# Kernel optimization log

Hardware: AMD Instinct MI355X
Metric: run time of the kernel (lower is better)

The kernel has to match this reference:

```python
import jax, jax.numpy as jnp
import numpy as np

B, S, E = 2, 2048, 1024
H = 16
D = E // H
LAYER_IDX = 2.0
MASKED_BIAS = -10000.0


def setup_inputs() -> dict:
    key = jax.random.key(0)
    k1, k2, k3 = jax.random.split(key, 3)
    hidden_state = jax.random.normal(k1, (B, S, E), dtype=jnp.float32)
    w_attn = jax.random.normal(k2, (E, 3 * E), dtype=jnp.float32) * 0.2
    b_attn = jnp.zeros((3 * E,), dtype=jnp.float32)
    w_proj = jax.random.normal(k3, (E, E), dtype=jnp.float32) * 0.2
    b_proj = jnp.zeros((E,), dtype=jnp.float32)
    return {"hidden_state": hidden_state, "w_attn": w_attn, "b_attn": b_attn,
            "w_proj": w_proj, "b_proj": b_proj}


def reference(hidden_state, w_attn, b_attn, w_proj, b_proj):
    b, s, e = hidden_state.shape
    # c_attn: Conv1D == x @ W + b, then split into q, k, v
    qkv = hidden_state @ w_attn + b_attn          # [b, s, 3E]
    q, k, v = jnp.split(qkv, 3, axis=-1)
    # split heads -> [b, H, s, D]
    def split_heads(t):
        return t.reshape(b, s, H, D).transpose(0, 2, 1, 3)
    q, k, v = split_heads(q), split_heads(k), split_heads(v)
    # QK^T scaled by sqrt(d_head) then by layer_idx
    scores = jnp.einsum("bhqd,bhkd->bhqk", q, k)
    scores = scores / jnp.asarray(D ** 0.5, scores.dtype)
    scores = scores / LAYER_IDX
    # causal mask with masked_bias fill (-10000.0), matching bias buffer slice
    causal = jnp.tril(jnp.ones((s, s), dtype=bool))  # [s, s]
    scores = jnp.where(causal[None, None, :, :], scores, jnp.asarray(MASKED_BIAS, scores.dtype))
    attn = jax.nn.softmax(scores, axis=-1)
    out = jnp.einsum("bhqk,bhkd->bhqd", attn, v)   # [b, H, s, D]
    # merge heads
    out = out.transpose(0, 2, 1, 3).reshape(b, s, e)
    # c_proj
    return out @ w_proj + b_proj
```

## Files before the change

### kernel.cpp

```cpp
#include <hip/hip_runtime.h>
#include <cstddef>
#include <cstdint>

#define B_DIM   2
#define S_LEN   2048
#define EMB     1024
#define NH      16
#define HD      64
#define QKV_N   3072
#define MROWS   (B_DIM * S_LEN)

using half8  = __attribute__((ext_vector_type(8))) _Float16;
using half4  = __attribute__((ext_vector_type(4))) _Float16;
using f32x4  = __attribute__((ext_vector_type(4))) float;

#if defined(__has_builtin)
#if __has_builtin(__builtin_amdgcn_global_load_lds)
#define HAS_GLL 1
#endif
#endif

__device__ __forceinline__ void stage16(const _Float16* g, _Float16* lds_base, int lane)
{
#ifdef HAS_GLL
    (void)lane;
    __builtin_amdgcn_global_load_lds(
        (const __attribute__((address_space(1))) unsigned int*)g,
        (__attribute__((address_space(3))) unsigned int*)lds_base, 16, 0, 0);
#else
    *(half8*)(lds_base + lane * 8) = *(const half8*)g;
#endif
}

__global__ __launch_bounds__(256)
void prep_all(const float* __restrict__ hidden, const float* __restrict__ w_attn,
              const float* __restrict__ w_proj, _Float16* __restrict__ hidden_h,
              _Float16* __restrict__ wattn_t, _Float16* __restrict__ wproj_t)
{
    const int bid = blockIdx.x, t = threadIdx.x;
    if (bid < 4096) {
        int i = bid * 1024 + t * 4;
        float4 v = *(const float4*)(hidden + i);
        half4 h = { (_Float16)v.x, (_Float16)v.y, (_Float16)v.z, (_Float16)v.w };
        *(half4*)(hidden_h + i) = h;
        return;
    }
    __shared__ float T[32][33];
    const float* W; _Float16* Wt; int N, bx, by;
    if (bid < 7168) {
        int t2 = bid - 4096; bx = t2 % 96; by = t2 / 96; W = w_attn; Wt = wattn_t; N = QKV_N;
    } else {
        int t3 = bid - 7168; bx = t3 & 31; by = t3 >> 5; W = w_proj; Wt = wproj_t; N = EMB;
    }
    const int n0 = bx * 32, k0 = by * 32;
    const int r = t >> 3, c4 = (t & 7) * 4;
    float4 w = *(const float4*)(W + (size_t)(k0 + r) * N + n0 + c4);
    T[r][c4 + 0] = w.x; T[r][c4 + 1] = w.y;
    T[r][c4 + 2] = w.z; T[r][c4 + 3] = w.w;
    __syncthreads();
    half4 h = { (_Float16)T[c4 + 0][r], (_Float16)T[c4 + 1][r],
                (_Float16)T[c4 + 2][r], (_Float16)T[c4 + 3][r] };
    *(half4*)(Wt + (size_t)(n0 + r) * EMB + k0 + c4) = h;
}

template <int MT, int MINW, bool OUT_F16, bool FUSE_VT>
__global__ __launch_bounds__(256, MINW)
void hgemm_lds(const _Float16* __restrict__ X, const _Float16* __restrict__ Wt,
               const float* __restrict__ bias, void* __restrict__ Cout,
               _Float16* __restrict__ vt, int M, int N, int K)
{
    constexpr int BM = MT * 32;
    constexpr int ACALLS = BM / 32;
    __shared__ _Float16 As[BM][64];
    __shared__ _Float16 Bs[128][64];

    const int tid  = threadIdx.x;
    const int wave = tid >> 6, lane = tid & 63;
    const int quad = lane >> 4, l15 = lane & 15;
    const int wm = (wave >> 1) * (MT * 16);
    const int wn = (wave & 1) * 64;
    const int m0 = blockIdx.y * BM, n0 = blockIdx.x * 128;

    const int srow = lane >> 3;
    const int scol = ((lane & 7) ^ srow) * 8;

    const _Float16* xg[ACALLS];
#pragma unroll
    for (int c = 0; c < ACALLS; ++c)
        xg[c] = X + (size_t)(m0 + wave * (BM / 4) + c * 8 + srow) * K + scol;
    const _Float16* wg[4];
#pragma unroll
    for (int c = 0; c < 4; ++c)
        wg[c] = Wt + (size_t)(n0 + wave * 32 + c * 8 + srow) * K + scol;

    f32x4 acc[MT][4] = {};
    const int sx = l15 & 7;

    for (int k0 = 0; k0 < K; k0 += 64) {
#pragma unroll
        for (int c = 0; c < ACALLS; ++c)
            stage16(xg[c] + k0, &As[wave * (BM / 4) + c * 8][0], lane);
#pragma unroll
        for (int c = 0; c < 4; ++c)
            stage16(wg[c] + k0, &Bs[wave * 32 + c * 8][0], lane);
        __syncthreads();

#pragma unroll
        for (int cc = 0; cc < 2; ++cc) {
            half8 af[MT], bf[4];
#pragma unroll
            for (int mt = 0; mt < MT; ++mt)
                af[mt] = *(const half8*)&As[wm + mt * 16 + l15][(((cc * 4 + quad) ^ sx)) * 8];
#pragma unroll
            for (int nt = 0; nt < 4; ++nt)
                bf[nt] = *(const half8*)&Bs[wn + nt * 16 + l15][(((cc * 4 + quad) ^ sx)) * 8];
#pragma unroll
            for (int mt = 0; mt < MT; ++mt)
#pragma unroll
                for (int nt = 0; nt < 4; ++nt)
                    acc[mt][nt] = __builtin_amdgcn_mfma_f32_16x16x32_f16(
                        af[mt], bf[nt], acc[mt][nt], 0, 0, 0);
        }
        __syncthreads();
    }

    if (FUSE_VT && n0 >= 2 * EMB) {
#pragma unroll
        for (int nt = 0; nt < 4; ++nt) {
            const int c  = n0 + wn + nt * 16 + l15;
            const float bv = bias[c];
            const int vcol = c - 2 * EMB;
            const int hh = vcol >> 6, dd = vcol & 63;
#pragma unroll
            for (int mt = 0; mt < MT; ++mt) {
                const int r = m0 + wm + mt * 16 + quad * 4;
                const int bb = r >> 11, ss = r & 2047;
                half4 o = { (_Float16)(acc[mt][nt][0] + bv), (_Float16)(acc[mt][nt][1] + bv),
                            (_Float16)(acc[mt][nt][2] + bv), (_Float16)(acc[mt][nt][3] + bv) };
                *(half4*)(vt + ((size_t)(bb * NH + hh) * HD + dd) * S_LEN + ss) = o;
            }
        }
        return;
    }

#pragma unroll
    for (int nt = 0; nt < 4; ++nt) {
        const int c = n0 + wn + nt * 16 + l15;
        const float bv = bias[c];
#pragma unroll
        for (int mt = 0; mt < MT; ++mt)
#pragma unroll
            for (int reg = 0; reg < 4; ++reg) {
                const int r = m0 + wm + mt * 16 + quad * 4 + reg;
                const float v = acc[mt][nt][reg] + bv;
                if (OUT_F16)
                    ((_Float16*)Cout)[(size_t)r * N + c] = (_Float16)v;
                else
                    ((float*)Cout)[(size_t)r * N + c] = v;
            }
    }
}

__global__ __launch_bounds__(256, 2)
void attn_fa_mfma7(const _Float16* __restrict__ qkv,
                   const _Float16* __restrict__ vt,
                   _Float16* __restrict__ outh)
{
    __shared__ _Float16 Ks[128][64];
    __shared__ _Float16 Vs[64][128];

    const int n   = blockIdx.x;
    const int xcd = n & 7, g = (n >> 3) & 3, j = n >> 5;
    const int bh  = xcd * 4 + g;
    const int qta = j, qtb = 31 - j;
    const int b = bh >> 4, h = bh & 15;

    const int tid  = threadIdx.x;
    const int wave = tid >> 6, lane = tid & 63;
    const int quad = lane >> 4, l15 = lane & 15;
    const size_t row0 = (size_t)b * S_LEN;

    const _Float16 qscale = (_Float16)0.0901684400555602f;
    half8 qfa[2], qfb[2];
    {
        const _Float16* qpa = qkv + (row0 + qta * 64 + wave * 16 + l15) * QKV_N + h * HD + quad * 8;
        const _Float16* qpb = qkv + (row0 + qtb * 64 + wave * 16 + l15) * QKV_N + h * HD + quad * 8;
#pragma unroll
        for (int c = 0; c < 2; ++c) {
            half8 qa = *(const half8*)(qpa + c * 32);
            half8 qb = *(const half8*)(qpb + c * 32);
#pragma unroll
            for (int j2 = 0; j2 < 8; ++j2) { qa[j2] *= qscale; qb[j2] *= qscale; }
            qfa[c] = qa; qfb[c] = qb;
        }
    }

    f32x4 o_a[4] = {}, o_b[4] = {};
    float m_a = -1e30f, l_a = 0.0f, m_b = -1e30f, l_b = 0.0f;

    const int ksrow = lane >> 3;
    const int kscol = ((lane & 7) ^ ksrow) * 8;
    const int vsrow = lane >> 4;
    const _Float16* vbase = vt + (size_t)bh * HD * S_LEN;
    const int sxk = l15 & 7;

    auto softmax_pack = [&](f32x4 (&st)[8], half4 (&pf)[8], float& m_i, float& l_i,
                            f32x4 (&o_acc)[4]) {
        float rm = fmaxf(fmaxf(st[0][0], st[0][1]), fmaxf(st[0][2], st[0][3]));
#pragma unroll
        for (int nt = 1; nt < 8; ++nt) {
            rm = fmaxf(rm, fmaxf(st[nt][0], st[nt][1]));
            rm = fmaxf(rm, fmaxf(st[nt][2], st[nt][3]));
        }
        rm = fmaxf(rm, __shfl_xor(rm, 16));
        rm = fmaxf(rm, __shfl_xor(rm, 32));
        const float mnew = fmaxf(m_i, rm);
        if (__ballot(mnew > m_i)) {
            const float alpha = __builtin_amdgcn_exp2f(m_i - mnew);
            l_i *= alpha;
#pragma unroll
            for (int dt = 0; dt < 4; ++dt)
#pragma unroll
                for (int reg = 0; reg < 4; ++reg) o_acc[dt][reg] *= alpha;
        }
        m_i = mnew;
        float rs = 0.0f;
#pragma unroll
        for (int nt = 0; nt < 8; ++nt) {
            float p0 = __builtin_amdgcn_exp2f(st[nt][0] - mnew);
            float p1 = __builtin_amdgcn_exp2f(st[nt][1] - mnew);
            float p2 = __builtin_amdgcn_exp2f(st[nt][2] - mnew);
            float p3 = __builtin_amdgcn_exp2f(st[nt][3] - mnew);
            rs += (p0 + p1) + (p2 + p3);
            pf[nt] = half4{ (_Float16)p0, (_Float16)p1, (_Float16)p2, (_Float16)p3 };
        }
        rs += __shfl_xor(rs, 16);
        rs += __shfl_xor(rs, 32);
        l_i += rs;
    };

    const int ktNa = (qta + 2) >> 1;
    const int ktNb = (qtb + 2) >> 1;

    for (int kt = 0; kt < ktNb; ++kt) {
        __syncthreads();
        {
            const _Float16* kbase = qkv + (row0 + kt * 128) * QKV_N + EMB + h * HD;
#pragma unroll
            for (int c = 0; c < 4; ++c) {
                const int r0 = wave * 32 + c * 8;
                stage16(kbase + (size_t)(r0 + ksrow) * QKV_N + kscol, &Ks[r0][0], lane);
            }
#pragma unroll
            for (int c = 0; c < 4; ++c) {
                const int r0 = wave * 16 + c * 4;
                const int sgv = ((lane & 15) ^ (c * 4 + vsrow)) * 8;
                stage16(vbase + (size_t)(r0 + vsrow) * S_LEN + kt * 128 + sgv, &Vs[r0][0], lane);
            }
        }
        __syncthreads();

        if (kt < ktNa) {
            f32x4 sa[8] = {}, sb[8] = {};
#pragma unroll
            for (int c = 0; c < 2; ++c)
#pragma unroll
                for (int nt = 0; nt < 8; ++nt) {
                    half8 kf = *(const half8*)&Ks[nt * 16 + l15][((c * 4 + quad) ^ sxk) * 8];
                    sa[nt] = __builtin_amdgcn_mfma_f32_16x16x32_f16(kf, qfa[c], sa[nt], 0, 0, 0);
                    sb[nt] = __builtin_amdgcn_mfma_f32_16x16x32_f16(kf, qfb[c], sb[nt], 0, 0, 0);
                }
            if (kt == ktNa - 1) {
                const int q = qta * 64 + wave * 16 + l15;
#pragma unroll
                for (int nt = 0; nt < 8; ++nt) {
                    const int ks = kt * 128 + nt * 16 + quad * 4;
#pragma unroll
                    for (int reg = 0; reg < 4; ++reg)
                        if (ks + reg > q) sa[nt][reg] = -1e30f;
                }
            }
            half4 pfa[8], pfb[8];
            softmax_pack(sa, pfa, m_a, l_a, o_a);
            softmax_pack(sb, pfb, m_b, l_b, o_b);
#pragma unroll
            for (int nt = 0; nt < 8; ++nt)
#pragma unroll
                for (int dt = 0; dt < 4; ++dt) {
                    const int pg = ((2 * nt + (quad >> 1)) ^ l15) * 8 + (quad & 1) * 4;
                    half4 vf = *(const half4*)&Vs[dt * 16 + l15][pg];
                    o_a[dt] = __builtin_amdgcn_mfma_f32_16x16x16f16(vf, pfa[nt], o_a[dt], 0, 0, 0);
                    o_b[dt] = __builtin_amdgcn_mfma_f32_16x16x16f16(vf, pfb[nt], o_b[dt], 0, 0, 0);
                }
        } else {
            f32x4 sb[8] = {};
#pragma unroll
            for (int c = 0; c < 2; ++c)
#pragma unroll
                for (int nt = 0; nt < 8; ++nt) {
                    half8 kf = *(const half8*)&Ks[nt * 16 + l15][((c * 4 + quad) ^ sxk) * 8];
                    sb[nt] = __builtin_amdgcn_mfma_f32_16x16x32_f16(kf, qfb[c], sb[nt], 0, 0, 0);
                }
            if (kt == ktNb - 1) {
                const int q = qtb * 64 + wave * 16 + l15;
#pragma unroll
                for (int nt = 0; nt < 8; ++nt) {
                    const int ks = kt * 128 + nt * 16 + quad * 4;
#pragma unroll
                    for (int reg = 0; reg < 4; ++reg)
                        if (ks + reg > q) sb[nt][reg] = -1e30f;
                }
            }
            half4 pfb[8];
            softmax_pack(sb, pfb, m_b, l_b, o_b);
#pragma unroll
            for (int nt = 0; nt < 8; ++nt)
#pragma unroll
                for (int dt = 0; dt < 4; ++dt) {
                    const int pg = ((2 * nt + (quad >> 1)) ^ l15) * 8 + (quad & 1) * 4;
                    half4 vf = *(const half4*)&Vs[dt * 16 + l15][pg];
                    o_b[dt] = __builtin_amdgcn_mfma_f32_16x16x16f16(vf, pfb[nt], o_b[dt], 0, 0, 0);
                }
        }
    }

    {
        const float inv = 1.0f / l_a;
        const size_t r = row0 + qta * 64 + wave * 16 + l15;
#pragma unroll
        for (int dt = 0; dt < 4; ++dt) {
            half4 o = { (_Float16)(o_a[dt][0] * inv), (_Float16)(o_a[dt][1] * inv),
                        (_Float16)(o_a[dt][2] * inv), (_Float16)(o_a[dt][3] * inv) };
            *(half4*)(outh + r * EMB + h * HD + dt * 16 + quad * 4) = o;
        }
    }
    {
        const float inv = 1.0f / l_b;
        const size_t r = row0 + qtb * 64 + wave * 16 + l15;
#pragma unroll
        for (int dt = 0; dt < 4; ++dt) {
            half4 o = { (_Float16)(o_b[dt][0] * inv), (_Float16)(o_b[dt][1] * inv),
                        (_Float16)(o_b[dt][2] * inv), (_Float16)(o_b[dt][3] * inv) };
            *(half4*)(outh + r * EMB + h * HD + dt * 16 + quad * 4) = o;
        }
    }
}

extern "C" void kernel_launch(void* const* d_in, const int* in_sizes, int n_in,
                              void* d_out, int out_size, void* d_ws, size_t ws_size,
                              hipStream_t stream)
{
    const float* hidden = (const float*)d_in[0];
    const float* w_attn = (const float*)d_in[1];
    const float* b_attn = (const float*)d_in[2];
    const float* w_proj = (const float*)d_in[3];
    const float* b_proj = (const float*)d_in[4];

    _Float16* hidden_h = (_Float16*)d_ws;
    _Float16* wattn_t  = hidden_h + (size_t)MROWS * EMB;
    _Float16* wproj_t  = wattn_t + (size_t)EMB * QKV_N;
    _Float16* qkv_h    = wproj_t + (size_t)EMB * EMB;
    _Float16* attn_h   = qkv_h + (size_t)MROWS * QKV_N;
    _Float16* vt       = attn_h + (size_t)MROWS * EMB;

    prep_all<<<8192, 256, 0, stream>>>(hidden, w_attn, w_proj,
                                       hidden_h, wattn_t, wproj_t);

    hgemm_lds<4, 3, true, true><<<dim3(QKV_N / 128, MROWS / 128), 256, 0, stream>>>(
        hidden_h, wattn_t, b_attn, qkv_h, vt, MROWS, QKV_N, EMB);

    attn_fa_mfma7<<<dim3(512), 256, 0, stream>>>(qkv_h, vt, attn_h);

    hgemm_lds<2, 4, false, false><<<dim3(EMB / 128, MROWS / 64), 256, 0, stream>>>(
        attn_h, wproj_t, b_proj, d_out, nullptr, MROWS, EMB, EMB);
}
```

Before: 170.3 us.

## Double-buffer K/V tiles in attention and raise wave priority around MFMA blocks

The attention kernel now keeps two LDS buffers each for K and V. It issues the global-to-LDS staging of tile kt+1 right after the barrier and before computing on tile kt, which removes one barrier per iteration and overlaps load latency with MFMA work. It also wraps the QK and PV MFMA loops in s_setprio to favour matrix-issuing waves. The cost is doubled LDS use, 64KB per block, which could limit occupancy, and correctness relies on the barrier draining the outstanding async loads.

```diff
diff --git a/kernel.cpp b/kernel.cpp
--- a/kernel.cpp
+++ b/kernel.cpp
@@ -162,12 +162,12 @@
 }
 
 __global__ __launch_bounds__(256, 2)
-void attn_fa_mfma7(const _Float16* __restrict__ qkv,
+void attn_fa_mfma8(const _Float16* __restrict__ qkv,
                    const _Float16* __restrict__ vt,
                    _Float16* __restrict__ outh)
 {
-    __shared__ _Float16 Ks[128][64];
-    __shared__ _Float16 Vs[64][128];
+    __shared__ _Float16 Ks[2][128][64];
+    __shared__ _Float16 Vs[2][64][128];
 
     const int n   = blockIdx.x;
     const int xcd = n & 7, g = (n >> 3) & 3, j = n >> 5;
@@ -203,6 +203,21 @@
     const int vsrow = lane >> 4;
     const _Float16* vbase = vt + (size_t)bh * HD * S_LEN;
     const int sxk = l15 & 7;
+
+    auto stage_tile = [&](int kt, int nb) {
+        const _Float16* kbase = qkv + (row0 + kt * 128) * QKV_N + EMB + h * HD;
+#pragma unroll
+        for (int c = 0; c < 4; ++c) {
+            const int r0 = wave * 32 + c * 8;
+            stage16(kbase + (size_t)(r0 + ksrow) * QKV_N + kscol, &Ks[nb][r0][0], lane);
+        }
+#pragma unroll
+        for (int c = 0; c < 4; ++c) {
+            const int r0 = wave * 16 + c * 4;
+            const int sgv = ((lane & 15) ^ (c * 4 + vsrow)) * 8;
+            stage16(vbase + (size_t)(r0 + vsrow) * S_LEN + kt * 128 + sgv, &Vs[nb][r0][0], lane);
+        }
+    };
 
     auto softmax_pack = [&](f32x4 (&st)[8], half4 (&pf)[8], float& m_i, float& l_i,
                             f32x4 (&o_acc)[4]) {
@@ -242,34 +257,26 @@
     const int ktNa = (qta + 2) >> 1;
     const int ktNb = (qtb + 2) >> 1;
 
+    stage_tile(0, 0);
+
     for (int kt = 0; kt < ktNb; ++kt) {
+        const int cur = kt & 1;
         __syncthreads();
-        {
-            const _Float16* kbase = qkv + (row0 + kt * 128) * QKV_N + EMB + h * HD;
-#pragma unroll
-            for (int c = 0; c < 4; ++c) {
-                const int r0 = wave * 32 + c * 8;
-                stage16(kbase + (size_t)(r0 + ksrow) * QKV_N + kscol, &Ks[r0][0], lane);
-            }
-#pragma unroll
-            for (int c = 0; c < 4; ++c) {
-                const int r0 = wave * 16 + c * 4;
-                const int sgv = ((lane & 15) ^ (c * 4 + vsrow)) * 8;
-                stage16(vbase + (size_t)(r0 + vsrow) * S_LEN + kt * 128 + sgv, &Vs[r0][0], lane);
-            }
-        }
-        __syncthreads();
+        if (kt + 1 < ktNb)
+            stage_tile(kt + 1, cur ^ 1);
 
         if (kt < ktNa) {
             f32x4 sa[8] = {}, sb[8] = {};
+            __builtin_amdgcn_s_setprio(1);
 #pragma unroll
             for (int c = 0; c < 2; ++c)
 #pragma unroll
                 for (int nt = 0; nt < 8; ++nt) {
-                    half8 kf = *(const half8*)&Ks[nt * 16 + l15][((c * 4 + quad) ^ sxk) * 8];
+                    half8 kf = *(const half8*)&Ks[cur][nt * 16 + l15][((c * 4 + quad) ^ sxk) * 8];
                     sa[nt] = __builtin_amdgcn_mfma_f32_16x16x32_f16(kf, qfa[c], sa[nt], 0, 0, 0);
                     sb[nt] = __builtin_amdgcn_mfma_f32_16x16x32_f16(kf, qfb[c], sb[nt], 0, 0, 0);
                 }
+            __builtin_amdgcn_s_setprio(0);
             if (kt == ktNa - 1) {
                 const int q = qta * 64 + wave * 16 + l15;
 #pragma unroll
@@ -283,24 +290,28 @@
             half4 pfa[8], pfb[8];
             softmax_pack(sa, pfa, m_a, l_a, o_a);
             softmax_pack(sb, pfb, m_b, l_b, o_b);
+            __builtin_amdgcn_s_setprio(1);
 #pragma unroll
             for (int nt = 0; nt < 8; ++nt)
 #pragma unroll
                 for (int dt = 0; dt < 4; ++dt) {
                     const int pg = ((2 * nt + (quad >> 1)) ^ l15) * 8 + (quad & 1) * 4;
-                    half4 vf = *(const half4*)&Vs[dt * 16 + l15][pg];
+                    half4 vf = *(const half4*)&Vs[cur][dt * 16 + l15][pg];
                     o_a[dt] = __builtin_amdgcn_mfma_f32_16x16x16f16(vf, pfa[nt], o_a[dt], 0, 0, 0);
                     o_b[dt] = __builtin_amdgcn_mfma_f32_16x16x16f16(vf, pfb[nt], o_b[dt], 0, 0, 0);
                 }
+            __builtin_amdgcn_s_setprio(0);
         } else {
             f32x4 sb[8] = {};
+            __builtin_amdgcn_s_setprio(1);
 #pragma unroll
             for (int c = 0; c < 2; ++c)
 #pragma unroll
                 for (int nt = 0; nt < 8; ++nt) {
-                    half8 kf = *(const half8*)&Ks[nt * 16 + l15][((c * 4 + quad) ^ sxk) * 8];
+                    half8 kf = *(const half8*)&Ks[cur][nt * 16 + l15][((c * 4 + quad) ^ sxk) * 8];
                     sb[nt] = __builtin_amdgcn_mfma_f32_16x16x32_f16(kf, qfb[c], sb[nt], 0, 0, 0);
                 }
+            __builtin_amdgcn_s_setprio(0);
             if (kt == ktNb - 1) {
                 const int q = qtb * 64 + wave * 16 + l15;
 #pragma unroll
@@ -313,14 +324,16 @@
             }
             half4 pfb[8];
             softmax_pack(sb, pfb, m_b, l_b, o_b);
+            __builtin_amdgcn_s_setprio(1);
 #pragma unroll
             for (int nt = 0; nt < 8; ++nt)
 #pragma unroll
                 for (int dt = 0; dt < 4; ++dt) {
                     const int pg = ((2 * nt + (quad >> 1)) ^ l15) * 8 + (quad & 1) * 4;
-                    half4 vf = *(const half4*)&Vs[dt * 16 + l15][pg];
+                    half4 vf = *(const half4*)&Vs[cur][dt * 16 + l15][pg];
                     o_b[dt] = __builtin_amdgcn_mfma_f32_16x16x16f16(vf, pfb[nt], o_b[dt], 0, 0, 0);
                 }
+            __builtin_amdgcn_s_setprio(0);
         }
     }
 
@@ -369,7 +382,7 @@
     hgemm_lds<4, 3, true, true><<<dim3(QKV_N / 128, MROWS / 128), 256, 0, stream>>>(
         hidden_h, wattn_t, b_attn, qkv_h, vt, MROWS, QKV_N, EMB);
 
-    attn_fa_mfma7<<<dim3(512), 256, 0, stream>>>(qkv_h, vt, attn_h);
+    attn_fa_mfma8<<<dim3(512), 256, 0, stream>>>(qkv_h, vt, attn_h);
 
     hgemm_lds<2, 4, false, false><<<dim3(EMB / 128, MROWS / 64), 256, 0, stream>>>(
         attn_h, wproj_t, b_proj, d_out, nullptr, MROWS, EMB, EMB);
```

New measurement: 173.9 us. +2.1%, slower.

## Double-buffer K/V LDS tiles in causal flash-attention kernel

Applied to the files above, without the earlier changes.

Adds a second pair of K/V shared-memory buffers and restructures the key-tile loop into a ping-pong schedule. The next tile's global-to-LDS staging is issued before the current tile's MFMA and softmax work, so load latency can hide behind compute, and one of the two barriers per tile is removed. The cost is twice the LDS per block (64 KB), which may limit occupancy, plus a slightly more complex loop with an early break for odd tile counts.

```diff
diff --git a/kernel.cpp b/kernel.cpp
--- a/kernel.cpp
+++ b/kernel.cpp
@@ -162,12 +162,14 @@
 }
 
 __global__ __launch_bounds__(256, 2)
-void attn_fa_mfma7(const _Float16* __restrict__ qkv,
+void attn_fa_mfma9(const _Float16* __restrict__ qkv,
                    const _Float16* __restrict__ vt,
                    _Float16* __restrict__ outh)
 {
-    __shared__ _Float16 Ks[128][64];
-    __shared__ _Float16 Vs[64][128];
+    __shared__ _Float16 Ks0[128][64];
+    __shared__ _Float16 Vs0[64][128];
+    __shared__ _Float16 Ks1[128][64];
+    __shared__ _Float16 Vs1[64][128];
 
     const int n   = blockIdx.x;
     const int xcd = n & 7, g = (n >> 3) & 3, j = n >> 5;
@@ -203,6 +205,24 @@
     const int vsrow = lane >> 4;
     const _Float16* vbase = vt + (size_t)bh * HD * S_LEN;
     const int sxk = l15 & 7;
+
+    const int ktNa = (qta + 2) >> 1;
+    const int ktNb = (qtb + 2) >> 1;
+
+    auto stage_tile = [&](int kt, _Float16 (&K)[128][64], _Float16 (&V)[64][128]) {
+        const _Float16* kbase = qkv + (row0 + kt * 128) * QKV_N + EMB + h * HD;
+#pragma unroll
+        for (int c = 0; c < 4; ++c) {
+            const int r0 = wave * 32 + c * 8;
+            stage16(kbase + (size_t)(r0 + ksrow) * QKV_N + kscol, &K[r0][0], lane);
+        }
+#pragma unroll
+        for (int c = 0; c < 4; ++c) {
+            const int r0 = wave * 16 + c * 4;
+            const int sgv = ((lane & 15) ^ (c * 4 + vsrow)) * 8;
+            stage16(vbase + (size_t)(r0 + vsrow) * S_LEN + kt * 128 + sgv, &V[r0][0], lane);
+        }
+    };
 
     auto softmax_pack = [&](f32x4 (&st)[8], half4 (&pf)[8], float& m_i, float& l_i,
                             f32x4 (&o_acc)[4]) {
@@ -239,34 +259,14 @@
         l_i += rs;
     };
 
-    const int ktNa = (qta + 2) >> 1;
-    const int ktNb = (qtb + 2) >> 1;
-
-    for (int kt = 0; kt < ktNb; ++kt) {
-        __syncthreads();
-        {
-            const _Float16* kbase = qkv + (row0 + kt * 128) * QKV_N + EMB + h * HD;
-#pragma unroll
-            for (int c = 0; c < 4; ++c) {
-                const int r0 = wave * 32 + c * 8;
-                stage16(kbase + (size_t)(r0 + ksrow) * QKV_N + kscol, &Ks[r0][0], lane);
-            }
-#pragma unroll
-            for (int c = 0; c < 4; ++c) {
-                const int r0 = wave * 16 + c * 4;
-                const int sgv = ((lane & 15) ^ (c * 4 + vsrow)) * 8;
-                stage16(vbase + (size_t)(r0 + vsrow) * S_LEN + kt * 128 + sgv, &Vs[r0][0], lane);
-            }
-        }
-        __syncthreads();
-
+    auto compute_tile = [&](int kt, _Float16 (&K)[128][64], _Float16 (&V)[64][128]) {
         if (kt < ktNa) {
             f32x4 sa[8] = {}, sb[8] = {};
 #pragma unroll
             for (int c = 0; c < 2; ++c)
 #pragma unroll
                 for (int nt = 0; nt < 8; ++nt) {
-                    half8 kf = *(const half8*)&Ks[nt * 16 + l15][((c * 4 + quad) ^ sxk) * 8];
+                    half8 kf = *(const half8*)&K[nt * 16 + l15][((c * 4 + quad) ^ sxk) * 8];
                     sa[nt] = __builtin_amdgcn_mfma_f32_16x16x32_f16(kf, qfa[c], sa[nt], 0, 0, 0);
                     sb[nt] = __builtin_amdgcn_mfma_f32_16x16x32_f16(kf, qfb[c], sb[nt], 0, 0, 0);
                 }
@@ -288,7 +288,7 @@
 #pragma unroll
                 for (int dt = 0; dt < 4; ++dt) {
                     const int pg = ((2 * nt + (quad >> 1)) ^ l15) * 8 + (quad & 1) * 4;
-                    half4 vf = *(const half4*)&Vs[dt * 16 + l15][pg];
+                    half4 vf = *(const half4*)&V[dt * 16 + l15][pg];
                     o_a[dt] = __builtin_amdgcn_mfma_f32_16x16x16f16(vf, pfa[nt], o_a[dt], 0, 0, 0);
                     o_b[dt] = __builtin_amdgcn_mfma_f32_16x16x16f16(vf, pfb[nt], o_b[dt], 0, 0, 0);
                 }
@@ -298,7 +298,7 @@
             for (int c = 0; c < 2; ++c)
 #pragma unroll
                 for (int nt = 0; nt < 8; ++nt) {
-                    half8 kf = *(const half8*)&Ks[nt * 16 + l15][((c * 4 + quad) ^ sxk) * 8];
+                    half8 kf = *(const half8*)&K[nt * 16 + l15][((c * 4 + quad) ^ sxk) * 8];
                     sb[nt] = __builtin_amdgcn_mfma_f32_16x16x32_f16(kf, qfb[c], sb[nt], 0, 0, 0);
                 }
             if (kt == ktNb - 1) {
@@ -318,10 +318,25 @@
 #pragma unroll
                 for (int dt = 0; dt < 4; ++dt) {
                     const int pg = ((2 * nt + (quad >> 1)) ^ l15) * 8 + (quad & 1) * 4;
-                    half4 vf = *(const half4*)&Vs[dt * 16 + l15][pg];
+                    half4 vf = *(const half4*)&V[dt * 16 + l15][pg];
                     o_b[dt] = __builtin_amdgcn_mfma_f32_16x16x16f16(vf, pfb[nt], o_b[dt], 0, 0, 0);
                 }
         }
+    };
+
+    stage_tile(0, Ks0, Vs0);
+
+    for (int kt = 0; kt < ktNb; kt += 2) {
+        __syncthreads();
+        if (kt + 1 < ktNb)
+            stage_tile(kt + 1, Ks1, Vs1);
+        compute_tile(kt, Ks0, Vs0);
+
+        if (kt + 1 >= ktNb) break;
+        __syncthreads();
+        if (kt + 2 < ktNb)
+            stage_tile(kt + 2, Ks0, Vs0);
+        compute_tile(kt + 1, Ks1, Vs1);
     }
 
     {
@@ -369,7 +384,7 @@
     hgemm_lds<4, 3, true, true><<<dim3(QKV_N / 128, MROWS / 128), 256, 0, stream>>>(
         hidden_h, wattn_t, b_attn, qkv_h, vt, MROWS, QKV_N, EMB);
 
-    attn_fa_mfma7<<<dim3(512), 256, 0, stream>>>(qkv_h, vt, attn_h);
+    attn_fa_mfma9<<<dim3(512), 256, 0, stream>>>(qkv_h, vt, attn_h);
 
     hgemm_lds<2, 4, false, false><<<dim3(EMB / 128, MROWS / 64), 256, 0, stream>>>(
         attn_h, wproj_t, b_proj, d_out, nullptr, MROWS, EMB, EMB);
```

Measured after the change: 170.6 us. About the same (+0.2%).

## Split paired-query-tile attention blocks into one tile per block with interleaved ordering

Applied to the files above, without the earlier changes.

The attention kernel previously had each block process two complementary query tiles (j and 31-j) sharing K/V loads. It now assigns one 64-row query tile per block, doubles the grid to 1024 blocks, and uses an interleaved tile ordering so heavy and light causal tiles are mixed across the dispatch. Launch bounds rise to 4 blocks per CU to raise occupancy now that register pressure is halved. The trade-off is that each K/V tile is loaded from global memory twice as often, since tiles no longer share staged K/V.

```diff
diff --git a/kernel.cpp b/kernel.cpp
--- a/kernel.cpp
+++ b/kernel.cpp
@@ -161,18 +161,19 @@
     }
 }
 
-__global__ __launch_bounds__(256, 2)
-void attn_fa_mfma7(const _Float16* __restrict__ qkv,
-                   const _Float16* __restrict__ vt,
-                   _Float16* __restrict__ outh)
+__global__ __launch_bounds__(256, 4)
+void attn_fa_mfma10(const _Float16* __restrict__ qkv,
+                    const _Float16* __restrict__ vt,
+                    _Float16* __restrict__ outh)
 {
     __shared__ _Float16 Ks[128][64];
     __shared__ _Float16 Vs[64][128];
 
     const int n   = blockIdx.x;
     const int xcd = n & 7, g = (n >> 3) & 3, j = n >> 5;
+    const int t   = j & 7, s = j >> 3;
+    const int qt  = (s & 1) ? (31 - 2 * t - (s >> 1)) : (2 * t + (s >> 1));
     const int bh  = xcd * 4 + g;
-    const int qta = j, qtb = 31 - j;
     const int b = bh >> 4, h = bh & 15;
 
     const int tid  = threadIdx.x;
@@ -181,22 +182,20 @@
     const size_t row0 = (size_t)b * S_LEN;
 
     const _Float16 qscale = (_Float16)0.0901684400555602f;
-    half8 qfa[2], qfb[2];
+    half8 qf[2];
     {
-        const _Float16* qpa = qkv + (row0 + qta * 64 + wave * 16 + l15) * QKV_N + h * HD + quad * 8;
-        const _Float16* qpb = qkv + (row0 + qtb * 64 + wave * 16 + l15) * QKV_N + h * HD + quad * 8;
+        const _Float16* qp = qkv + (row0 + qt * 64 + wave * 16 + l15) * QKV_N + h * HD + quad * 8;
 #pragma unroll
         for (int c = 0; c < 2; ++c) {
-            half8 qa = *(const half8*)(qpa + c * 32);
-            half8 qb = *(const half8*)(qpb + c * 32);
-#pragma unroll
-            for (int j2 = 0; j2 < 8; ++j2) { qa[j2] *= qscale; qb[j2] *= qscale; }
-            qfa[c] = qa; qfb[c] = qb;
-        }
-    }
-
-    f32x4 o_a[4] = {}, o_b[4] = {};
-    float m_a = -1e30f, l_a = 0.0f, m_b = -1e30f, l_b = 0.0f;
+            half8 q = *(const half8*)(qp + c * 32);
+#pragma unroll
+            for (int j2 = 0; j2 < 8; ++j2) q[j2] *= qscale;
+            qf[c] = q;
+        }
+    }
+
+    f32x4 o_acc[4] = {};
+    float m_i = -1e30f, l_i = 0.0f;
 
     const int ksrow = lane >> 3;
     const int kscol = ((lane & 7) ^ ksrow) * 8;
@@ -204,45 +203,9 @@
     const _Float16* vbase = vt + (size_t)bh * HD * S_LEN;
     const int sxk = l15 & 7;
 
-    auto softmax_pack = [&](f32x4 (&st)[8], half4 (&pf)[8], float& m_i, float& l_i,
-                            f32x4 (&o_acc)[4]) {
-        float rm = fmaxf(fmaxf(st[0][0], st[0][1]), fmaxf(st[0][2], st[0][3]));
-#pragma unroll
-        for (int nt = 1; nt < 8; ++nt) {
-            rm = fmaxf(rm, fmaxf(st[nt][0], st[nt][1]));
-            rm = fmaxf(rm, fmaxf(st[nt][2], st[nt][3]));
-        }
-        rm = fmaxf(rm, __shfl_xor(rm, 16));
-        rm = fmaxf(rm, __shfl_xor(rm, 32));
-        const float mnew = fmaxf(m_i, rm);
-        if (__ballot(mnew > m_i)) {
-            const float alpha = __builtin_amdgcn_exp2f(m_i - mnew);
-            l_i *= alpha;
-#pragma unroll
-            for (int dt = 0; dt < 4; ++dt)
-#pragma unroll
-                for (int reg = 0; reg < 4; ++reg) o_acc[dt][reg] *= alpha;
-        }
-        m_i = mnew;
-        float rs = 0.0f;
-#pragma unroll
-        for (int nt = 0; nt < 8; ++nt) {
-            float p0 = __builtin_amdgcn_exp2f(st[nt][0] - mnew);
-            float p1 = __builtin_amdgcn_exp2f(st[nt][1] - mnew);
-            float p2 = __builtin_amdgcn_exp2f(st[nt][2] - mnew);
-            float p3 = __builtin_amdgcn_exp2f(st[nt][3] - mnew);
-            rs += (p0 + p1) + (p2 + p3);
-            pf[nt] = half4{ (_Float16)p0, (_Float16)p1, (_Float16)p2, (_Float16)p3 };
-        }
-        rs += __shfl_xor(rs, 16);
-        rs += __shfl_xor(rs, 32);
-        l_i += rs;
-    };
-
-    const int ktNa = (qta + 2) >> 1;
-    const int ktNb = (qtb + 2) >> 1;
-
-    for (int kt = 0; kt < ktNb; ++kt) {
+    const int ktN = (qt + 2) >> 1;
+
+    for (int kt = 0; kt < ktN; ++kt) {
         __syncthreads();
         {
             const _Float16* kbase = qkv + (row0 + kt * 128) * QKV_N + EMB + h * HD;
@@ -260,87 +223,77 @@
         }
         __syncthreads();
 
-        if (kt < ktNa) {
-            f32x4 sa[8] = {}, sb[8] = {};
-#pragma unroll
-            for (int c = 0; c < 2; ++c)
-#pragma unroll
-                for (int nt = 0; nt < 8; ++nt) {
-                    half8 kf = *(const half8*)&Ks[nt * 16 + l15][((c * 4 + quad) ^ sxk) * 8];
-                    sa[nt] = __builtin_amdgcn_mfma_f32_16x16x32_f16(kf, qfa[c], sa[nt], 0, 0, 0);
-                    sb[nt] = __builtin_amdgcn_mfma_f32_16x16x32_f16(kf, qfb[c], sb[nt], 0, 0, 0);
-                }
-            if (kt == ktNa - 1) {
-                const int q = qta * 64 + wave * 16 + l15;
-#pragma unroll
-                for (int nt = 0; nt < 8; ++nt) {
-                    const int ks = kt * 128 + nt * 16 + quad * 4;
-#pragma unroll
-                    for (int reg = 0; reg < 4; ++reg)
-                        if (ks + reg > q) sa[nt][reg] = -1e30f;
-                }
-            }
-            half4 pfa[8], pfb[8];
-            softmax_pack(sa, pfa, m_a, l_a, o_a);
-            softmax_pack(sb, pfb, m_b, l_b, o_b);
-#pragma unroll
-            for (int nt = 0; nt < 8; ++nt)
-#pragma unroll
-                for (int dt = 0; dt < 4; ++dt) {
-                    const int pg = ((2 * nt + (quad >> 1)) ^ l15) * 8 + (quad & 1) * 4;
-                    half4 vf = *(const half4*)&Vs[dt * 16 + l15][pg];
-                    o_a[dt] = __builtin_amdgcn_mfma_f32_16x16x16f16(vf, pfa[nt], o_a[dt], 0, 0, 0);
-                    o_b[dt] = __builtin_amdgcn_mfma_f32_16x16x16f16(vf, pfb[nt], o_b[dt], 0, 0, 0);
-                }
-        } else {
-            f32x4 sb[8] = {};
-#pragma unroll
-            for (int c = 0; c < 2; ++c)
-#pragma unroll
-                for (int nt = 0; nt < 8; ++nt) {
-                    half8 kf = *(const half8*)&Ks[nt * 16 + l15][((c * 4 + quad) ^ sxk) * 8];
-                    sb[nt] = __builtin_amdgcn_mfma_f32_16x16x32_f16(kf, qfb[c], sb[nt], 0, 0, 0);
-                }
-            if (kt == ktNb - 1) {
-                const int q = qtb * 64 + wave * 16 + l15;
-#pragma unroll
-                for (int nt = 0; nt < 8; ++nt) {
-                    const int ks = kt * 128 + nt * 16 + quad * 4;
-#pragma unroll
-                    for (int reg = 0; reg < 4; ++reg)
-                        if (ks + reg > q) sb[nt][reg] = -1e30f;
-                }
-            }
-            half4 pfb[8];
-            softmax_pack(sb, pfb, m_b, l_b, o_b);
-#pragma unroll
-            for (int nt = 0; nt < 8; ++nt)
-#pragma unroll
-                for (int dt = 0; dt < 4; ++dt) {
-                    const int pg = ((2 * nt + (quad >> 1)) ^ l15) * 8 + (quad & 1) * 4;
-                    half4 vf = *(const half4*)&Vs[dt * 16 + l15][pg];
-                    o_b[dt] = __builtin_amdgcn_mfma_f32_16x16x16f16(vf, pfb[nt], o_b[dt], 0, 0, 0);
-                }
-        }
+        f32x4 st[8] = {};
+#pragma unroll
+        for (int c = 0; c < 2; ++c)
+#pragma unroll
+            for (int nt = 0; nt < 8; ++nt) {
+                half8 kf = *(const half8*)&Ks[nt * 16 + l15][((c * 4 + quad) ^ sxk) * 8];
+                st[nt] = __builtin_amdgcn_mfma_f32_16x16x32_f16(kf, qf[c], st[nt], 0, 0, 0);
+            }
+        if (kt == ktN - 1) {
+            const int q = qt * 64 + wave * 16 + l15;
+#pragma unroll
+            for (int nt = 0; nt < 8; ++nt) {
+                const int ks = kt * 128 + nt * 16 + quad * 4;
+#pragma unroll
+                for (int reg = 0; reg < 4; ++reg)
+                    if (ks + reg > q) st[nt][reg] = -1e30f;
+            }
+        }
+
+        half4 pf[8];
+        {
+            float rm = fmaxf(fmaxf(st[0][0], st[0][1]), fmaxf(st[0][2], st[0][3]));
+#pragma unroll
+            for (int nt = 1; nt < 8; ++nt) {
+                rm = fmaxf(rm, fmaxf(st[nt][0], st[nt][1]));
+                rm = fmaxf(rm, fmaxf(st[nt][2], st[nt][3]));
+            }
+            rm = fmaxf(rm, __shfl_xor(rm, 16));
+            rm = fmaxf(rm, __shfl_xor(rm, 32));
+            const float mnew = fmaxf(m_i, rm);
+            if (__ballot(mnew > m_i)) {
+                const float alpha = __builtin_amdgcn_exp2f(m_i - mnew);
+                l_i *= alpha;
+#pragma unroll
+                for (int dt = 0; dt < 4; ++dt)
+#pragma unroll
+                    for (int reg = 0; reg < 4; ++reg) o_acc[dt][reg] *= alpha;
+            }
+            m_i = mnew;
+            float rs = 0.0f;
+#pragma unroll
+            for (int nt = 0; nt < 8; ++nt) {
+                float p0 = __builtin_amdgcn_exp2f(st[nt][0] - mnew);
+                float p1 = __builtin_amdgcn_exp2f(st[nt][1] - mnew);
+                float p2 = __builtin_amdgcn_exp2f(st[nt][2] - mnew);
+                float p3 = __builtin_amdgcn_exp2f(st[nt][3] - mnew);
+                rs += (p0 + p1) + (p2 + p3);
+                pf[nt] = half4{ (_Float16)p0, (_Float16)p1, (_Float16)p2, (_Float16)p3 };
+            }
+            rs += __shfl_xor(rs, 16);
+            rs += __shfl_xor(rs, 32);
+            l_i += rs;
+        }
+
+#pragma unroll
+        for (int nt = 0; nt < 8; ++nt)
+#pragma unroll
+            for (int dt = 0; dt < 4; ++dt) {
+                const int pg = ((2 * nt + (quad >> 1)) ^ l15) * 8 + (quad & 1) * 4;
+                half4 vf = *(const half4*)&Vs[dt * 16 + l15][pg];
+                o_acc[dt] = __builtin_amdgcn_mfma_f32_16x16x16f16(vf, pf[nt], o_acc[dt], 0, 0, 0);
+            }
     }
 
     {
-        const float inv = 1.0f / l_a;
-        const size_t r = row0 + qta * 64 + wave * 16 + l15;
+        const float inv = 1.0f / l_i;
+        const size_t r = row0 + qt * 64 + wave * 16 + l15;
 #pragma unroll
         for (int dt = 0; dt < 4; ++dt) {
-            half4 o = { (_Float16)(o_a[dt][0] * inv), (_Float16)(o_a[dt][1] * inv),
-                        (_Float16)(o_a[dt][2] * inv), (_Float16)(o_a[dt][3] * inv) };
-            *(half4*)(outh + r * EMB + h * HD + dt * 16 + quad * 4) = o;
-        }
-    }
-    {
-        const float inv = 1.0f / l_b;
-        const size_t r = row0 + qtb * 64 + wave * 16 + l15;
-#pragma unroll
-        for (int dt = 0; dt < 4; ++dt) {
-            half4 o = { (_Float16)(o_b[dt][0] * inv), (_Float16)(o_b[dt][1] * inv),
-                        (_Float16)(o_b[dt][2] * inv), (_Float16)(o_b[dt][3] * inv) };
+            half4 o = { (_Float16)(o_acc[dt][0] * inv), (_Float16)(o_acc[dt][1] * inv),
+                        (_Float16)(o_acc[dt][2] * inv), (_Float16)(o_acc[dt][3] * inv) };
             *(half4*)(outh + r * EMB + h * HD + dt * 16 + quad * 4) = o;
         }
     }
@@ -369,7 +322,7 @@
     hgemm_lds<4, 3, true, true><<<dim3(QKV_N / 128, MROWS / 128), 256, 0, stream>>>(
         hidden_h, wattn_t, b_attn, qkv_h, vt, MROWS, QKV_N, EMB);
 
-    attn_fa_mfma7<<<dim3(512), 256, 0, stream>>>(qkv_h, vt, attn_h);
+    attn_fa_mfma10<<<dim3(1024), 256, 0, stream>>>(qkv_h, vt, attn_h);
 
     hgemm_lds<2, 4, false, false><<<dim3(EMB / 128, MROWS / 64), 256, 0, stream>>>(
         attn_h, wproj_t, b_proj, d_out, nullptr, MROWS, EMB, EMB);
```

Result: slower. 177.5 us (+4.3%).
